# Kernel tuning notes

Hardware: AMD Instinct MI355X
Metric: run time of the kernel (lower is better)

Reference implementation:

```python
import jax, jax.numpy as jnp
import numpy as np

E, H_HEADS, WS = 512, 16, 8
HEAD_D = E // H_HEADS
LN_EPS = 1e-5


def layernorm(x, g, b):
    mu = jnp.mean(x, axis=-1, keepdims=True)
    var = jnp.mean((x - mu) ** 2, axis=-1, keepdims=True)
    return (x - mu) / jnp.sqrt(var + LN_EPS) * g + b


def setup_inputs() -> dict:
    key = jax.random.key(0)
    ks = jax.random.split(key, 10)
    s = 0.02
    return {
        "x": jax.random.normal(ks[0], (4, 4096, E), jnp.float32),
        "in_proj_w": jax.random.normal(ks[1], (3 * E, E), jnp.float32) * s,
        "in_proj_b": jnp.zeros((3 * E,), jnp.float32),
        "out_w": jax.random.normal(ks[2], (E, E), jnp.float32) * s,
        "out_b": jnp.zeros((E,), jnp.float32),
        "ln1_g": jnp.ones((E,), jnp.float32),
        "ln1_b": jnp.zeros((E,), jnp.float32),
        "w1": jax.random.normal(ks[3], (4 * E, E), jnp.float32) * s,
        "b1": jnp.zeros((4 * E,), jnp.float32),
        "w2": jax.random.normal(ks[4], (E, 4 * E), jnp.float32) * s,
        "b2": jnp.zeros((E,), jnp.float32),
        "ln2_g": jnp.ones((E,), jnp.float32),
        "ln2_b": jnp.zeros((E,), jnp.float32),
        "num_patches_h": 64,
        "num_patches_w": 64,
    }


def reference(x, in_proj_w, in_proj_b, out_w, out_b, ln1_g, ln1_b,
              w1, b1, w2, b2, ln2_g, ln2_b, num_patches_h, num_patches_w):
    B, P, _ = x.shape
    Hp, Wp = num_patches_h, num_patches_w  # 64 divisible by WS -> no padding branch
    nwh, nww = Hp // WS, Wp // WS
    # window partition: (B, Hp, Wp, E) -> (B*nW, WS*WS, E)
    xw = x.reshape(B, nwh, WS, nww, WS, E).transpose(0, 1, 3, 2, 4, 5)
    xw = xw.reshape(B * nwh * nww, WS * WS, E)
    # nn.MultiheadAttention default batch_first=False: axis0 is SEQ (L=B*nW),
    # axis1 is BATCH (N=WS*WS). Reproduce that literal semantics.
    L, N = xw.shape[0], xw.shape[1]
    qkv = xw @ in_proj_w.T + in_proj_b          # (L, N, 3E)
    q, k, v = jnp.split(qkv, 3, axis=-1)
    qh = q.reshape(L, N, H_HEADS, HEAD_D)
    kh = k.reshape(L, N, H_HEADS, HEAD_D)
    vh = v.reshape(L, N, H_HEADS, HEAD_D)
    scale = 1.0 / np.sqrt(HEAD_D)
    scores = jnp.einsum('lnhd,mnhd->nhlm', qh, kh) * scale  # (N, h, L, L)
    attn = jax.nn.softmax(scores, axis=-1)
    o = jnp.einsum('nhlm,mnhd->lnhd', attn, vh).reshape(L, N, E)
    attn_out = o @ out_w.T + out_b
    y = layernorm(xw + attn_out, ln1_g, ln1_b)
    ffn = jax.nn.gelu(y @ w1.T + b1, approximate=False) @ w2.T + b2
    y = layernorm(y + ffn, ln2_g, ln2_b)
    # window unpartition
    y = y.reshape(B, nwh, nww, WS, WS, E).transpose(0, 1, 3, 2, 4, 5)
    return y.reshape(B, Hp * Wp, E)[:, :P, :]
```

## Files before the change

kernel.cpp:

```cpp
#include <hip/hip_runtime.h>
#include <cmath>


typedef _Float16 half8 __attribute__((ext_vector_type(8)));
typedef _Float16 half4v __attribute__((ext_vector_type(4)));
typedef float f32x4 __attribute__((ext_vector_type(4)));

#define GLOBAL_AS(p) ((const __attribute__((address_space(1))) void*)(p))
#define LDS_AS(p) ((__attribute__((address_space(3))) void*)(p))

__device__ __forceinline__ void gload_lds16(const _Float16* g, _Float16* l) {
  __builtin_amdgcn_global_load_lds(GLOBAL_AS(g), LDS_AS(l), 16, 0, 0);
}

__device__ __forceinline__ float wave_sum(float v) {
#pragma unroll
  for (int off = 32; off > 0; off >>= 1) v += __shfl_xor(v, off, 64);
  return v;
}

__device__ __forceinline__ float gelu_fast(float x) {
  const float y = 1.5957691216057308f * (x + 0.044715f * x * x * x);
  const float e = __expf(y);
  const float t = 1.0f - 2.0f / (e + 1.0f);
  return 0.5f * x * (1.0f + t);
}

__global__ __launch_bounds__(256) void castw_kernel(const float* __restrict__ s,
                                                    _Float16* __restrict__ d, int n) {
  const int i = (blockIdx.x * 256 + threadIdx.x) * 4;
  if (i >= n) return;
  const float4 v = *(const float4*)&s[i];
  half4v o;
  o[0] = (_Float16)v.x; o[1] = (_Float16)v.y; o[2] = (_Float16)v.z; o[3] = (_Float16)v.w;
  *(half4v*)&d[i] = o;
}

__global__ __launch_bounds__(256) void gather_x_kernel(const float* __restrict__ x,
                                                       _Float16* __restrict__ xw) {
  const int idx = blockIdx.x * 256 + threadIdx.x;
  const int t = idx >> 6;
  const int e0 = (idx & 63) << 3;
  const int l = t >> 6, n = t & 63;
  const int bb = l >> 6, wh = (l >> 3) & 7, ww = l & 7;
  const int pi = n >> 3, pj = n & 7;
  const int xrow = (bb * 4096 + (wh * 8 + pi) * 64 + (ww * 8 + pj)) * 512;
  const float4 a = *(const float4*)&x[xrow + e0];
  const float4 b = *(const float4*)&x[xrow + e0 + 4];
  half8 o;
  o[0] = (_Float16)a.x; o[1] = (_Float16)a.y; o[2] = (_Float16)a.z; o[3] = (_Float16)a.w;
  o[4] = (_Float16)b.x; o[5] = (_Float16)b.y; o[6] = (_Float16)b.z; o[7] = (_Float16)b.w;
  *(half8*)&xw[t * 512 + e0] = o;
}

template <int EPI, int WM, int WN, int MREP>
__global__ __launch_bounds__(WM * WN * 64, 2) void gemmp_kernel(
    const _Float16* __restrict__ A, const _Float16* __restrict__ B,
    const float* __restrict__ bias, _Float16* __restrict__ C,
    int M, int N, int K) {
  constexpr int BM = WM * MREP * 16;
  constexpr int BN = WN * 64;
  constexpr int NW = WM * WN;
  constexpr int AH = BM * 32;
  constexpr int BH = BN * 32;
  constexpr int MH = MREP / 2;
  __shared__ _Float16 L[2][2 * AH + 2 * BH];

  const int tid = threadIdx.x;
  const int lane = tid & 63, wave = tid >> 6;
  const int wr = wave / WN, wc = wave % WN;
  const int lr = lane & 15, g = lane >> 4;
  const int bm = blockIdx.x, bn = blockIdx.y;

  const int srow = lane >> 2;
  const int sslot = lane & 3;
  const int sswz = ((sslot ^ (srow & 3)) << 3);
  const _Float16* Ap = A + (size_t)(bm * BM) * K;
  const _Float16* Bp = B + (size_t)(bn * BN) * K;
  const size_t a0 = (size_t)(wave * 32 + srow) * K + sswz;
  const size_t a1 = a0 + (size_t)16 * K;

  auto stageA = [&](int b, int tt, int hk) {
    const _Float16* src = Ap + tt * 64 + hk * 32;
    _Float16* dst = &L[b][hk * AH] + wave * 1024;
    gload_lds16(src + a0, dst);
    gload_lds16(src + a1, dst + 512);
  };
  auto stageB = [&](int b, int tt, int hk) {
    const _Float16* src = Bp + tt * 64 + hk * 32;
    _Float16* dst = &L[b][2 * AH + hk * BH] + wave * 1024;
    gload_lds16(src + a0, dst);
    gload_lds16(src + a1, dst + 512);
  };

  const int fsw = ((g ^ (lr & 3)) << 3);
  int aoffs[MREP], boffs[4];
#pragma unroll
  for (int m = 0; m < MREP; ++m) aoffs[m] = (wr * MREP * 16 + m * 16 + lr) * 32 + fsw;
#pragma unroll
  for (int n = 0; n < 4; ++n) boffs[n] = (wc * 64 + n * 16 + lr) * 32 + fsw;

  f32x4 acc[MREP][4] = {};
  const int NT = K >> 6;

  stageA(0, 0, 0); stageB(0, 0, 0); stageA(0, 0, 1); stageB(0, 0, 1);
  stageA(1, 1, 0); stageB(1, 1, 0);
  asm volatile("s_waitcnt vmcnt(4)" ::: "memory");
  asm volatile("s_barrier" ::: "memory");

  for (int t = 0; t < NT; ++t) {
    const int p = t & 1, q = p ^ 1;
    const _Float16* Lp = &L[p][0];
    half8 af[MH], bf[4];
#pragma unroll
    for (int m = 0; m < MH; ++m) af[m] = *(const half8*)&Lp[aoffs[m]];
#pragma unroll
    for (int n = 0; n < 4; ++n) bf[n] = *(const half8*)&Lp[2 * AH + boffs[n]];
    if (t + 1 < NT) stageA(q, t + 1, 1);
    asm volatile("s_barrier" ::: "memory");
    __builtin_amdgcn_s_setprio(1);
#pragma unroll
    for (int m = 0; m < MH; ++m)
#pragma unroll
      for (int n = 0; n < 4; ++n)
        acc[m][n] = __builtin_amdgcn_mfma_f32_16x16x32_f16(af[m], bf[n], acc[m][n], 0, 0, 0);
    __builtin_amdgcn_s_setprio(0);
    asm volatile("s_barrier" ::: "memory");
#pragma unroll
    for (int m = 0; m < MH; ++m) af[m] = *(const half8*)&Lp[aoffs[MH + m]];
    if (t + 1 < NT) stageB(q, t + 1, 1);
    asm volatile("s_barrier" ::: "memory");
    __builtin_amdgcn_s_setprio(1);
#pragma unroll
    for (int m = 0; m < MH; ++m)
#pragma unroll
      for (int n = 0; n < 4; ++n)
        acc[MH + m][n] = __builtin_amdgcn_mfma_f32_16x16x32_f16(af[m], bf[n], acc[MH + m][n], 0, 0, 0);
    __builtin_amdgcn_s_setprio(0);
    asm volatile("s_barrier" ::: "memory");
#pragma unroll
    for (int m = 0; m < MH; ++m) af[m] = *(const half8*)&Lp[AH + aoffs[m]];
#pragma unroll
    for (int n = 0; n < 4; ++n) bf[n] = *(const half8*)&Lp[2 * AH + BH + boffs[n]];
    if (t + 2 < NT) stageA(p, t + 2, 0);
    asm volatile("s_barrier" ::: "memory");
    __builtin_amdgcn_s_setprio(1);
#pragma unroll
    for (int m = 0; m < MH; ++m)
#pragma unroll
      for (int n = 0; n < 4; ++n)
        acc[m][n] = __builtin_amdgcn_mfma_f32_16x16x32_f16(af[m], bf[n], acc[m][n], 0, 0, 0);
    __builtin_amdgcn_s_setprio(0);
    asm volatile("s_barrier" ::: "memory");
#pragma unroll
    for (int m = 0; m < MH; ++m) af[m] = *(const half8*)&Lp[AH + aoffs[MH + m]];
    if (t + 2 < NT) stageB(p, t + 2, 0);
    asm volatile("s_barrier" ::: "memory");
    __builtin_amdgcn_s_setprio(1);
#pragma unroll
    for (int m = 0; m < MH; ++m)
#pragma unroll
      for (int n = 0; n < 4; ++n)
        acc[MH + m][n] = __builtin_amdgcn_mfma_f32_16x16x32_f16(af[m], bf[n], acc[MH + m][n], 0, 0, 0);
    __builtin_amdgcn_s_setprio(0);
    if (t + 1 < NT) {
      if (t + 2 < NT) asm volatile("s_waitcnt vmcnt(4)" ::: "memory");
      else            asm volatile("s_waitcnt vmcnt(0)" ::: "memory");
    }
    asm volatile("s_barrier" ::: "memory");
  }

  float bsv[4];
#pragma unroll
  for (int n = 0; n < 4; ++n) bsv[n] = bias[bn * BN + wc * 64 + n * 16 + lr];
  _Float16* Lc = &L[0][0] + wave * (MREP * 16 * 64);
#pragma unroll
  for (int m = 0; m < MREP; ++m)
#pragma unroll
    for (int n = 0; n < 4; ++n)
#pragma unroll
      for (int r = 0; r < 4; ++r) {
        float v = acc[m][n][r] + bsv[n];
        if (EPI == 1) v = gelu_fast(v);
        const int row = m * 16 + g * 4 + r;
        const int col = n * 16 + lr;
        Lc[row * 64 + (col ^ ((row & 7) << 3))] = (_Float16)v;
      }
  const int rrow = lane >> 3, slot = lane & 7;
  const int growb = bm * BM + wr * MREP * 16;
  const int gcol = bn * BN + wc * 64 + slot * 8;
#pragma unroll
  for (int blk = 0; blk < MREP * 2; ++blk) {
    const int row = blk * 8 + rrow;
    const half8 vv = *(const half8*)&Lc[row * 64 + ((slot ^ (row & 7)) << 3)];
    *(half8*)&C[(size_t)(growb + row) * N + gcol] = vv;
  }
}

__global__ __launch_bounds__(256) void attn_kernel(const _Float16* __restrict__ qkv,
                                                   _Float16* __restrict__ o_out) {
  const int n = blockIdx.x & 63;
  const int h = blockIdx.x >> 6;
  __shared__ _Float16 Ksh[256 * 40];
  __shared__ _Float16 Vt[32 * 264];
  __shared__ _Float16 Pw[4 * 64 * 72];
  const int tid = threadIdx.x;
  const int wq = tid >> 6, lane = tid & 63;
  const int lr = lane & 15, g = lane >> 4;
  const int hq = h * 32;

#pragma unroll
  for (int pass = 0; pass < 4; ++pass) {
    const int e = pass * 2048 + tid * 8;
    const int m = e >> 5, d = e & 31;
    const int base = (m * 64 + n) * 1536 + hq;
    const half8 k8 = *(const half8*)&qkv[base + 512 + d];
    const half8 v8 = *(const half8*)&qkv[base + 1024 + d];
    *(half8*)&Ksh[m * 40 + d] = k8;
#pragma unroll
    for (int j = 0; j < 8; ++j) Vt[(d + j) * 264 + m] = v8[j];
  }
  half8 qf[4];
#pragma unroll
  for (int qt = 0; qt < 4; ++qt) {
    const int qg = wq * 64 + qt * 16 + lr;
    qf[qt] = *(const half8*)&qkv[(qg * 64 + n) * 1536 + hq + g * 8];
  }
  __syncthreads();

  f32x4 o[4][2] = {};
  float den[4] = {0.f, 0.f, 0.f, 0.f};
  const float scale = 0.17677669529663687f;
  _Float16* P = &Pw[wq * (64 * 72)];

  for (int it = 0; it < 4; ++it) {
    const int k0 = it * 64;
#pragma unroll
    for (int qt = 0; qt < 4; ++qt) {
#pragma unroll
      for (int kt = 0; kt < 4; ++kt) {
        const half8 kf = *(const half8*)&Ksh[(k0 + kt * 16 + lr) * 40 + g * 8];
        const f32x4 z = {0.f, 0.f, 0.f, 0.f};
        f32x4 st = __builtin_amdgcn_mfma_f32_16x16x32_f16(kf, qf[qt], z, 0, 0, 0);
        const float p0 = __expf(st[0] * scale);
        const float p1 = __expf(st[1] * scale);
        const float p2 = __expf(st[2] * scale);
        const float p3 = __expf(st[3] * scale);
        den[qt] += (p0 + p1) + (p2 + p3);
        half4v w;
        w[0] = (_Float16)p0; w[1] = (_Float16)p1;
        w[2] = (_Float16)p2; w[3] = (_Float16)p3;
        *(half4v*)&P[(qt * 16 + lr) * 72 + kt * 16 + g * 4] = w;
      }
    }
    __syncthreads();
#pragma unroll
    for (int qt = 0; qt < 4; ++qt) {
#pragma unroll
      for (int ks = 0; ks < 2; ++ks) {
        const half8 pf = *(const half8*)&P[(qt * 16 + lr) * 72 + ks * 32 + g * 8];
#pragma unroll
        for (int dt = 0; dt < 2; ++dt) {
          const half8 vf = *(const half8*)&Vt[(dt * 16 + lr) * 264 + k0 + ks * 32 + g * 8];
          o[qt][dt] = __builtin_amdgcn_mfma_f32_16x16x32_f16(pf, vf, o[qt][dt], 0, 0, 0);
        }
      }
    }
    __syncthreads();
  }

#pragma unroll
  for (int qt = 0; qt < 4; ++qt) {
    float dq = den[qt];
    dq += __shfl_xor(dq, 16);
    dq += __shfl_xor(dq, 32);
    const float inv = 1.0f / dq;
#pragma unroll
    for (int r = 0; r < 4; ++r) {
      const float invr = __shfl(inv, g * 4 + r);
      const int qg = wq * 64 + qt * 16 + g * 4 + r;
      const int obase = (qg * 64 + n) * 512 + hq;
#pragma unroll
      for (int dt = 0; dt < 2; ++dt)
        o_out[obase + dt * 16 + lr] = (_Float16)(o[qt][dt][r] * invr);
    }
  }
}

template <int FINAL>
__global__ __launch_bounds__(256) void ln_kernel(
    const float* __restrict__ res32, const _Float16* __restrict__ add16,
    const float* __restrict__ g, const float* __restrict__ b,
    float* __restrict__ out32, _Float16* __restrict__ out16) {
  const int t = blockIdx.x * 4 + (threadIdx.x >> 6);
  const int lane = threadIdx.x & 63;
  const int e0 = lane << 3;
  const int l = t >> 6, n = t & 63;
  const int bb = l >> 6, wh = (l >> 3) & 7, ww = l & 7;
  const int pi = n >> 3, pj = n & 7;
  const int xrow = (bb * 4096 + (wh * 8 + pi) * 64 + (ww * 8 + pj)) * 512;
  const int trow = t * 512;
  const int rbase = (FINAL ? trow : xrow) + e0;
  const float4 ra = *(const float4*)&res32[rbase];
  const float4 rb = *(const float4*)&res32[rbase + 4];
  const half8 a8 = *(const half8*)&add16[trow + e0];
  float v[8];
  v[0] = ra.x + (float)a8[0]; v[1] = ra.y + (float)a8[1];
  v[2] = ra.z + (float)a8[2]; v[3] = ra.w + (float)a8[3];
  v[4] = rb.x + (float)a8[4]; v[5] = rb.y + (float)a8[5];
  v[6] = rb.z + (float)a8[6]; v[7] = rb.w + (float)a8[7];
  float s = 0.f;
#pragma unroll
  for (int e = 0; e < 8; ++e) s += v[e];
  s = wave_sum(s);
  const float mu = s * (1.0f / 512.0f);
  float vs = 0.f;
#pragma unroll
  for (int e = 0; e < 8; ++e) { const float d = v[e] - mu; vs += d * d; }
  vs = wave_sum(vs);
  const float rstd = rsqrtf(vs * (1.0f / 512.0f) + 1e-5f);
  const float4 g1 = *(const float4*)&g[e0];
  const float4 g2 = *(const float4*)&g[e0 + 4];
  const float4 b1 = *(const float4*)&b[e0];
  const float4 b2 = *(const float4*)&b[e0 + 4];
  float y[8];
  y[0] = (v[0] - mu) * rstd * g1.x + b1.x; y[1] = (v[1] - mu) * rstd * g1.y + b1.y;
  y[2] = (v[2] - mu) * rstd * g1.z + b1.z; y[3] = (v[3] - mu) * rstd * g1.w + b1.w;
  y[4] = (v[4] - mu) * rstd * g2.x + b2.x; y[5] = (v[5] - mu) * rstd * g2.y + b2.y;
  y[6] = (v[6] - mu) * rstd * g2.z + b2.z; y[7] = (v[7] - mu) * rstd * g2.w + b2.w;
  if (FINAL) {
    *(float4*)&out32[xrow + e0] = make_float4(y[0], y[1], y[2], y[3]);
    *(float4*)&out32[xrow + e0 + 4] = make_float4(y[4], y[5], y[6], y[7]);
  } else {
    *(float4*)&out32[trow + e0] = make_float4(y[0], y[1], y[2], y[3]);
    *(float4*)&out32[trow + e0 + 4] = make_float4(y[4], y[5], y[6], y[7]);
    half8 o16;
#pragma unroll
    for (int e = 0; e < 8; ++e) o16[e] = (_Float16)y[e];
    *(half8*)&out16[trow + e0] = o16;
  }
}

extern "C" void kernel_launch(void* const* d_in, const int* in_sizes, int n_in,
                              void* d_out, int out_size, void* d_ws, size_t ws_size,
                              hipStream_t stream) {
  const float* x    = (const float*)d_in[0];
  const float* ipw  = (const float*)d_in[1];
  const float* ipb  = (const float*)d_in[2];
  const float* outw = (const float*)d_in[3];
  const float* outb = (const float*)d_in[4];
  const float* ln1g = (const float*)d_in[5];
  const float* ln1b = (const float*)d_in[6];
  const float* w1   = (const float*)d_in[7];
  const float* b1   = (const float*)d_in[8];
  const float* w2   = (const float*)d_in[9];
  const float* b2   = (const float*)d_in[10];
  const float* ln2g = (const float*)d_in[11];
  const float* ln2b = (const float*)d_in[12];
  float* out = (float*)d_out;
  char* ws = (char*)d_ws;

  _Float16* wqkv_h = (_Float16*)(ws + 0);
  _Float16* wout_h = (_Float16*)(ws + 1572864);
  _Float16* w1_h   = (_Float16*)(ws + 2097152);
  _Float16* w2_h   = (_Float16*)(ws + 4194304);
  _Float16* xw_h   = (_Float16*)(ws + 6291456);
  _Float16* qkv_h  = (_Float16*)(ws + 23068672);
  _Float16* attn_h = (_Float16*)(ws + 90177536);
  _Float16* ao_h   = (_Float16*)(ws + 106954752);
  float*    y32    = (float*)(ws + 123731968);
  _Float16* h_h = qkv_h;
  _Float16* f_h = attn_h;
  _Float16* y16 = xw_h;

  castw_kernel<<<768, 256, 0, stream>>>(ipw, wqkv_h, 786432);
  castw_kernel<<<256, 256, 0, stream>>>(outw, wout_h, 262144);
  castw_kernel<<<1024, 256, 0, stream>>>(w1, w1_h, 1048576);
  castw_kernel<<<1024, 256, 0, stream>>>(w2, w2_h, 1048576);
  gather_x_kernel<<<4096, 256, 0, stream>>>(x, xw_h);
  gemmp_kernel<0, 2, 4, 8><<<dim3(64, 6), 512, 0, stream>>>(xw_h, wqkv_h, ipb, qkv_h, 16384, 1536, 512);
  attn_kernel<<<1024, 256, 0, stream>>>(qkv_h, attn_h);
  gemmp_kernel<0, 2, 2, 4><<<dim3(128, 4), 256, 0, stream>>>(attn_h, wout_h, outb, ao_h, 16384, 512, 512);
  ln_kernel<0><<<4096, 256, 0, stream>>>(x, ao_h, ln1g, ln1b, y32, y16);
  gemmp_kernel<1, 2, 4, 8><<<dim3(64, 8), 512, 0, stream>>>(y16, w1_h, b1, h_h, 16384, 2048, 512);
  gemmp_kernel<0, 2, 2, 4><<<dim3(128, 4), 256, 0, stream>>>(h_h, w2_h, b2, f_h, 16384, 512, 2048);
  ln_kernel<1><<<4096, 256, 0, stream>>>(y32, f_h, ln2g, ln2b, out, nullptr);
}
```

Measured before the change: 246.9 us.

## Simplify GEMM pipeline to full-K64 tile stages and merge weight casts

Replaces the GEMM's split-half-K staging, which used many interleaved barriers, with a simpler double-buffered scheme. Each stage loads a full 64-wide K tile into an XOR-swizzled LDS layout, and each iteration needs only one or two barriers. Also merges the four weight-cast launches into a single kernel that picks its source by block index. This cuts barrier and launch overhead, but global-to-LDS prefetch now overlaps with MFMA work less finely.

Measured after the change: 229.0 us. 1.08x faster.

```diff
diff --git a/kernel.cpp b/kernel.cpp
--- a/kernel.cpp
+++ b/kernel.cpp
@@ -26,10 +26,18 @@
   return 0.5f * x * (1.0f + t);
 }
 
-__global__ __launch_bounds__(256) void castw_kernel(const float* __restrict__ s,
-                                                    _Float16* __restrict__ d, int n) {
-  const int i = (blockIdx.x * 256 + threadIdx.x) * 4;
-  if (i >= n) return;
+__global__ __launch_bounds__(256) void castw4_kernel(
+    const float* __restrict__ s0, _Float16* __restrict__ d0,
+    const float* __restrict__ s1, _Float16* __restrict__ d1,
+    const float* __restrict__ s2, _Float16* __restrict__ d2,
+    const float* __restrict__ s3, _Float16* __restrict__ d3) {
+  int b = blockIdx.x;
+  const float* s; _Float16* d;
+  if (b < 768) { s = s0; d = d0; }
+  else if (b < 1024) { s = s1; d = d1; b -= 768; }
+  else if (b < 2048) { s = s2; d = d2; b -= 1024; }
+  else { s = s3; d = d3; b -= 2048; }
+  const int i = (b * 256 + threadIdx.x) * 4;
   const float4 v = *(const float4*)&s[i];
   half4v o;
   o[0] = (_Float16)v.x; o[1] = (_Float16)v.y; o[2] = (_Float16)v.z; o[3] = (_Float16)v.w;
@@ -54,121 +62,95 @@
 }
 
 template <int EPI, int WM, int WN, int MREP>
-__global__ __launch_bounds__(WM * WN * 64, 2) void gemmp_kernel(
+__global__ __launch_bounds__(WM * WN * 64, 2) void gemm_kernel(
     const _Float16* __restrict__ A, const _Float16* __restrict__ B,
     const float* __restrict__ bias, _Float16* __restrict__ C,
     int M, int N, int K) {
   constexpr int BM = WM * MREP * 16;
   constexpr int BN = WN * 64;
   constexpr int NW = WM * WN;
-  constexpr int AH = BM * 32;
-  constexpr int BH = BN * 32;
-  constexpr int MH = MREP / 2;
-  __shared__ _Float16 L[2][2 * AH + 2 * BH];
-
-  const int tid = threadIdx.x;
-  const int lane = tid & 63, wave = tid >> 6;
+  constexpr int TA = BM * 64, TB = BN * 64;
+  constexpr int ALW = BM / (8 * NW);
+  constexpr int BLW = BN / (8 * NW);
+  __shared__ _Float16 L[2][TA + TB];
+
+  const int tid = threadIdx.x, lane = tid & 63, wave = tid >> 6;
   const int wr = wave / WN, wc = wave % WN;
   const int lr = lane & 15, g = lane >> 4;
   const int bm = blockIdx.x, bn = blockIdx.y;
 
-  const int srow = lane >> 2;
-  const int sslot = lane & 3;
-  const int sswz = ((sslot ^ (srow & 3)) << 3);
-  const _Float16* Ap = A + (size_t)(bm * BM) * K;
-  const _Float16* Bp = B + (size_t)(bn * BN) * K;
-  const size_t a0 = (size_t)(wave * 32 + srow) * K + sswz;
-  const size_t a1 = a0 + (size_t)16 * K;
-
-  auto stageA = [&](int b, int tt, int hk) {
-    const _Float16* src = Ap + tt * 64 + hk * 32;
-    _Float16* dst = &L[b][hk * AH] + wave * 1024;
-    gload_lds16(src + a0, dst);
-    gload_lds16(src + a1, dst + 512);
+  const int scol = ((lane & 7) ^ (lane >> 3)) << 3;
+  const int srow = lane >> 3;
+  const _Float16* Ap = A + (size_t)(bm * BM) * K + scol;
+  const _Float16* Bp = B + (size_t)(bn * BN) * K + scol;
+
+  auto stage = [&](int b, int tt) {
+    const int koff = tt * 64;
+#pragma unroll
+    for (int i = 0; i < ALW; ++i) {
+      const int r0 = wave * (8 * ALW) + i * 8;
+      gload_lds16(Ap + (size_t)(r0 + srow) * K + koff, &L[b][r0 * 64]);
+    }
+#pragma unroll
+    for (int i = 0; i < BLW; ++i) {
+      const int r0 = wave * (8 * BLW) + i * 8;
+      gload_lds16(Bp + (size_t)(r0 + srow) * K + koff, &L[b][TA + r0 * 64]);
+    }
   };
-  auto stageB = [&](int b, int tt, int hk) {
-    const _Float16* src = Bp + tt * 64 + hk * 32;
-    _Float16* dst = &L[b][2 * AH + hk * BH] + wave * 1024;
-    gload_lds16(src + a0, dst);
-    gload_lds16(src + a1, dst + 512);
-  };
-
-  const int fsw = ((g ^ (lr & 3)) << 3);
-  int aoffs[MREP], boffs[4];
-#pragma unroll
-  for (int m = 0; m < MREP; ++m) aoffs[m] = (wr * MREP * 16 + m * 16 + lr) * 32 + fsw;
-#pragma unroll
-  for (int n = 0; n < 4; ++n) boffs[n] = (wc * 64 + n * 16 + lr) * 32 + fsw;
+
+  int aoff[2][MREP], boff[2][4];
+#pragma unroll
+  for (int kk = 0; kk < 2; ++kk) {
+#pragma unroll
+    for (int m = 0; m < MREP; ++m) {
+      const int row = wr * MREP * 16 + m * 16 + lr;
+      aoff[kk][m] = row * 64 + (((kk * 4 + g) ^ (row & 7)) << 3);
+    }
+#pragma unroll
+    for (int n = 0; n < 4; ++n) {
+      const int row = wc * 64 + n * 16 + lr;
+      boff[kk][n] = TA + row * 64 + (((kk * 4 + g) ^ (row & 7)) << 3);
+    }
+  }
 
   f32x4 acc[MREP][4] = {};
   const int NT = K >> 6;
 
-  stageA(0, 0, 0); stageB(0, 0, 0); stageA(0, 0, 1); stageB(0, 0, 1);
-  stageA(1, 1, 0); stageB(1, 1, 0);
-  asm volatile("s_waitcnt vmcnt(4)" ::: "memory");
+  stage(0, 0);
+  stage(1, 1);
+  asm volatile("s_waitcnt vmcnt(8)" ::: "memory");
   asm volatile("s_barrier" ::: "memory");
 
   for (int t = 0; t < NT; ++t) {
-    const int p = t & 1, q = p ^ 1;
+    const int p = t & 1;
     const _Float16* Lp = &L[p][0];
-    half8 af[MH], bf[4];
-#pragma unroll
-    for (int m = 0; m < MH; ++m) af[m] = *(const half8*)&Lp[aoffs[m]];
-#pragma unroll
-    for (int n = 0; n < 4; ++n) bf[n] = *(const half8*)&Lp[2 * AH + boffs[n]];
-    if (t + 1 < NT) stageA(q, t + 1, 1);
+#pragma unroll
+    for (int kk = 0; kk < 2; ++kk) {
+      half8 af[MREP], bf[4];
+#pragma unroll
+      for (int m = 0; m < MREP; ++m) af[m] = *(const half8*)&Lp[aoff[kk][m]];
+#pragma unroll
+      for (int n = 0; n < 4; ++n) bf[n] = *(const half8*)&Lp[boff[kk][n]];
+      __builtin_amdgcn_s_setprio(1);
+#pragma unroll
+      for (int m = 0; m < MREP; ++m)
+#pragma unroll
+        for (int n = 0; n < 4; ++n)
+          acc[m][n] = __builtin_amdgcn_mfma_f32_16x16x32_f16(af[m], bf[n], acc[m][n], 0, 0, 0);
+      __builtin_amdgcn_s_setprio(0);
+    }
+    asm volatile("s_waitcnt lgkmcnt(0)" ::: "memory");
     asm volatile("s_barrier" ::: "memory");
-    __builtin_amdgcn_s_setprio(1);
-#pragma unroll
-    for (int m = 0; m < MH; ++m)
-#pragma unroll
-      for (int n = 0; n < 4; ++n)
-        acc[m][n] = __builtin_amdgcn_mfma_f32_16x16x32_f16(af[m], bf[n], acc[m][n], 0, 0, 0);
-    __builtin_amdgcn_s_setprio(0);
-    asm volatile("s_barrier" ::: "memory");
-#pragma unroll
-    for (int m = 0; m < MH; ++m) af[m] = *(const half8*)&Lp[aoffs[MH + m]];
-    if (t + 1 < NT) stageB(q, t + 1, 1);
-    asm volatile("s_barrier" ::: "memory");
-    __builtin_amdgcn_s_setprio(1);
-#pragma unroll
-    for (int m = 0; m < MH; ++m)
-#pragma unroll
-      for (int n = 0; n < 4; ++n)
-        acc[MH + m][n] = __builtin_amdgcn_mfma_f32_16x16x32_f16(af[m], bf[n], acc[MH + m][n], 0, 0, 0);
-    __builtin_amdgcn_s_setprio(0);
-    asm volatile("s_barrier" ::: "memory");
-#pragma unroll
-    for (int m = 0; m < MH; ++m) af[m] = *(const half8*)&Lp[AH + aoffs[m]];
-#pragma unroll
-    for (int n = 0; n < 4; ++n) bf[n] = *(const half8*)&Lp[2 * AH + BH + boffs[n]];
-    if (t + 2 < NT) stageA(p, t + 2, 0);
-    asm volatile("s_barrier" ::: "memory");
-    __builtin_amdgcn_s_setprio(1);
-#pragma unroll
-    for (int m = 0; m < MH; ++m)
-#pragma unroll
-      for (int n = 0; n < 4; ++n)
-        acc[m][n] = __builtin_amdgcn_mfma_f32_16x16x32_f16(af[m], bf[n], acc[m][n], 0, 0, 0);
-    __builtin_amdgcn_s_setprio(0);
-    asm volatile("s_barrier" ::: "memory");
-#pragma unroll
-    for (int m = 0; m < MH; ++m) af[m] = *(const half8*)&Lp[AH + aoffs[MH + m]];
-    if (t + 2 < NT) stageB(p, t + 2, 0);
-    asm volatile("s_barrier" ::: "memory");
-    __builtin_amdgcn_s_setprio(1);
-#pragma unroll
-    for (int m = 0; m < MH; ++m)
-#pragma unroll
-      for (int n = 0; n < 4; ++n)
-        acc[MH + m][n] = __builtin_amdgcn_mfma_f32_16x16x32_f16(af[m], bf[n], acc[MH + m][n], 0, 0, 0);
-    __builtin_amdgcn_s_setprio(0);
+    if (t + 2 < NT) stage(p, t + 2);
     if (t + 1 < NT) {
-      if (t + 2 < NT) asm volatile("s_waitcnt vmcnt(4)" ::: "memory");
+      if (t + 2 < NT) asm volatile("s_waitcnt vmcnt(8)" ::: "memory");
       else            asm volatile("s_waitcnt vmcnt(0)" ::: "memory");
-    }
-    asm volatile("s_barrier" ::: "memory");
-  }
+      asm volatile("s_barrier" ::: "memory");
+    }
+  }
+
+  asm volatile("s_waitcnt lgkmcnt(0)" ::: "memory");
+  asm volatile("s_barrier" ::: "memory");
 
   float bsv[4];
 #pragma unroll
@@ -373,16 +355,13 @@
   _Float16* f_h = attn_h;
   _Float16* y16 = xw_h;
 
-  castw_kernel<<<768, 256, 0, stream>>>(ipw, wqkv_h, 786432);
-  castw_kernel<<<256, 256, 0, stream>>>(outw, wout_h, 262144);
-  castw_kernel<<<1024, 256, 0, stream>>>(w1, w1_h, 1048576);
-  castw_kernel<<<1024, 256, 0, stream>>>(w2, w2_h, 1048576);
+  castw4_kernel<<<3072, 256, 0, stream>>>(ipw, wqkv_h, outw, wout_h, w1, w1_h, w2, w2_h);
   gather_x_kernel<<<4096, 256, 0, stream>>>(x, xw_h);
-  gemmp_kernel<0, 2, 4, 8><<<dim3(64, 6), 512, 0, stream>>>(xw_h, wqkv_h, ipb, qkv_h, 16384, 1536, 512);
+  gemm_kernel<0, 2, 4, 8><<<dim3(64, 6), 512, 0, stream>>>(xw_h, wqkv_h, ipb, qkv_h, 16384, 1536, 512);
   attn_kernel<<<1024, 256, 0, stream>>>(qkv_h, attn_h);
-  gemmp_kernel<0, 2, 2, 4><<<dim3(128, 4), 256, 0, stream>>>(attn_h, wout_h, outb, ao_h, 16384, 512, 512);
+  gemm_kernel<0, 2, 2, 4><<<dim3(128, 4), 256, 0, stream>>>(attn_h, wout_h, outb, ao_h, 16384, 512, 512);
   ln_kernel<0><<<4096, 256, 0, stream>>>(x, ao_h, ln1g, ln1b, y32, y16);
-  gemmp_kernel<1, 2, 4, 8><<<dim3(64, 8), 512, 0, stream>>>(y16, w1_h, b1, h_h, 16384, 2048, 512);
-  gemmp_kernel<0, 2, 2, 4><<<dim3(128, 4), 256, 0, stream>>>(h_h, w2_h, b2, f_h, 16384, 512, 2048);
+  gemm_kernel<1, 2, 4, 8><<<dim3(64, 8), 512, 0, stream>>>(y16, w1_h, b1, h_h, 16384, 2048, 512);
+  gemm_kernel<0, 2, 2, 4><<<dim3(128, 4), 256, 0, stream>>>(h_h, w2_h, b2, f_h, 16384, 512, 2048);
   ln_kernel<1><<<4096, 256, 0, stream>>>(y32, f_h, ln2g, ln2b, out, nullptr);
 }
```
